# Kernel tuning notes

Measured on AMD Instinct MI355X. Metric: run time of the kernel, lower is better.

## Reference

```python
import jax, jax.numpy as jnp
import numpy as np


def setup_inputs() -> dict:
    key = jax.random.key(0)
    ks = jax.random.split(key, 5)
    B, T, S, D = 4, 32, 320, 768
    return {
        "x": jax.random.normal(ks[0], (B, T, S, D), dtype=jnp.float32),
        "qkv_w": jax.random.normal(ks[1], (D, 3 * D), dtype=jnp.float32) * 0.02,
        "qkv_b": jax.random.normal(ks[2], (3 * D,), dtype=jnp.float32) * 0.02,
        "out_w": jax.random.normal(ks[3], (D, D), dtype=jnp.float32) * 0.02,
        "out_b": jax.random.normal(ks[4], (D,), dtype=jnp.float32) * 0.02,
        "n_latents": 64,
        "n_heads": 12,
    }


def reference(x, qkv_w, qkv_b, out_w, out_b, n_latents, n_heads):
    B, T, S, D = x.shape
    H = n_heads
    hd = D // H
    scale = 1.0 / jnp.sqrt(jnp.asarray(hd, dtype=x.dtype))

    # qkv projection: [B,T,S,3D]
    qkv = jnp.einsum('btsd,de->btse', x, qkv_w) + qkv_b
    q, k, v = jnp.split(qkv, 3, axis=-1)
    # [B,T,S,H,hd]
    q = q.reshape(B, T, S, H, hd)
    k = k.reshape(B, T, S, H, hd)
    v = v.reshape(B, T, S, H, hd)

    # block-sparse mask: latent queries (rows < n_latents) cannot attend to
    # patch keys (cols >= n_latents); everything else allowed
    rows = jnp.arange(S) < n_latents          # latent query rows
    cols = jnp.arange(S) >= n_latents         # patch key cols
    allow = ~(rows[:, None] & cols[None, :])  # [S,S] bool

    # attention scores [B,T,H,Sq,Sk]
    scores = jnp.einsum('btqhd,btkhd->bthqk', q, k) * scale
    scores = jnp.where(allow, scores, -jnp.inf)
    attn = jax.nn.softmax(scores, axis=-1)

    y = jnp.einsum('bthqk,btkhd->btqhd', attn, v).reshape(B, T, S, D)
    return jnp.einsum('btsd,de->btse', y, out_w) + out_b
```

## Files before the change

kernel.cpp:

```cpp
#include <hip/hip_runtime.h>

typedef __attribute__((ext_vector_type(8))) short bf16x8;
typedef __attribute__((ext_vector_type(4))) float f32x4;
typedef __attribute__((ext_vector_type(16))) float f32x16;
typedef __attribute__((address_space(1))) void gvoid_t;
typedef __attribute__((address_space(3))) void lvoid_t;

#define DEVI __device__ __forceinline__
#define SB __builtin_amdgcn_sched_barrier(0)

DEVI unsigned short f2bf(float f) {
    unsigned int u = __builtin_bit_cast(unsigned int, f);
    u += 0x7fffu + ((u >> 16) & 1u);
    return (unsigned short)(u >> 16);
}

DEVI unsigned cvt_pk_bf16(float a, float b) {
    unsigned r;
    asm("v_cvt_pk_bf16_f32 %0, %1, %2" : "=v"(r) : "v"(a), "v"(b));
    return r;
}

DEVI f32x4 mfma16(bf16x8 a, bf16x8 b, f32x4 c) {
    return __builtin_amdgcn_mfma_f32_16x16x32_bf16(a, b, c, 0, 0, 0);
}

__global__ void k_convert(const float* __restrict__ in, unsigned short* __restrict__ out, int n8) {
    int i = blockIdx.x * 256 + threadIdx.x;
    if (i >= n8) return;
    const float4* p = (const float4*)in + (size_t)i * 2;
    float4 a = p[0], b = p[1];
    uint4 o;
    o.x = f2bf(a.x) | ((unsigned)f2bf(a.y) << 16);
    o.y = f2bf(a.z) | ((unsigned)f2bf(a.w) << 16);
    o.z = f2bf(b.x) | ((unsigned)f2bf(b.y) << 16);
    o.w = f2bf(b.z) | ((unsigned)f2bf(b.w) << 16);
    *((uint4*)out + i) = o;
}

__global__ void k_transpose(const float* __restrict__ w, unsigned short* __restrict__ wt, int K, int N) {
    __shared__ float tile[32][33];
    int n0 = blockIdx.x * 32, k0 = blockIdx.y * 32;
    int tx = threadIdx.x, ty = threadIdx.y;
#pragma unroll
    for (int r = 0; r < 32; r += 8)
        tile[ty + r][tx] = w[(size_t)(k0 + ty + r) * N + n0 + tx];
    __syncthreads();
#pragma unroll
    for (int r = 0; r < 32; r += 8)
        wt[(size_t)(n0 + ty + r) * K + k0 + tx] = f2bf(tile[tx][ty + r]);
}

__global__ __launch_bounds__(256) void k_kpack(const unsigned short* __restrict__ qkv,
                                               unsigned short* __restrict__ kp) {
    int bht = blockIdx.x;
    int t = bht % 10, bh = bht / 10;
    int h = bh % 12, bt = bh / 12;
    int c = threadIdx.x >> 6, l = threadIdx.x & 63;
    const unsigned short* src = qkv + (size_t)(bt * 320 + t * 32 + (l & 31)) * 2304
                                + 768 + h * 64 + c * 16 + (l >> 5) * 8;
    uint4 v = *(const uint4*)src;
    *(uint4*)(kp + ((size_t)bht * 4 + c) * 512 + l * 8) = v;
}

template <bool OUT_BF16>
__global__ __launch_bounds__(512, 2) void k_gemm256(const unsigned short* __restrict__ A,
                                                    const unsigned short* __restrict__ Bt,
                                                    const float* __restrict__ bias,
                                                    void* __restrict__ out,
                                                    int M, int N, int K) {
    __shared__ unsigned short smem[65536];

    const int tid = threadIdx.x;
    const int nwg = gridDim.x, bid = blockIdx.x;
    const int q8 = nwg >> 3, r8 = nwg & 7;
    const int xcd = bid & 7, lid = bid >> 3;
    const int swz = ((xcd < r8) ? xcd * (q8 + 1) : r8 * (q8 + 1) + (xcd - r8) * q8) + lid;
    const int ntn = N >> 8;
    const int bm = swz / ntn, bn = swz % ntn;

    const int lane = tid & 63, wid = tid >> 6;
    const int wr = wid >> 2, wc = wid & 3;
    const int lr = lane & 15, lg = lane >> 4;
    const int cswz = (lr & 7) << 3;
    const int col0 = (lg * 8) ^ cswz;

    const int NT = K >> 6;

    const int srowl = tid >> 3;
    const int scole = ((tid & 7) ^ (srowl & 7)) << 3;
    const unsigned short* aSrc = A  + (size_t)(bm * 256 + srowl) * K + scole;
    const unsigned short* bSrc = Bt + (size_t)(bn * 256 + srowl) * K + scole;

#define STG(matOff, srcBase, qq, koff, bufw)                                              \
    __builtin_amdgcn_global_load_lds((gvoid_t*)((srcBase) + (size_t)(qq) * 64 * K + (koff)), \
        (lvoid_t*)(smem + (matOff) + (bufw) * 16384 + (qq) * 4096 + tid * 8), 16, 0, 0)
#define LDA(mf, base, rowoff, kk) \
    *(const bf16x8*)((base) + ((rowoff) + (mf) * 16 + lr) * 64 + (col0 ^ ((kk) * 32)))

    f32x4 acc[8][4];
#pragma unroll
    for (int i = 0; i < 8; ++i)
#pragma unroll
        for (int j = 0; j < 4; ++j) acc[i][j] = (f32x4){0.f, 0.f, 0.f, 0.f};

    {
        const int k1 = (NT > 1) ? 64 : 0;
        STG(0, aSrc, 0, 0, 0); STG(0, aSrc, 1, 0, 0); STG(0, aSrc, 2, 0, 0); STG(0, aSrc, 3, 0, 0);
        STG(32768, bSrc, 0, 0, 0); STG(32768, bSrc, 1, 0, 0); STG(32768, bSrc, 2, 0, 0); STG(32768, bSrc, 3, 0, 0);
        STG(0, aSrc, 0, k1, 1); STG(0, aSrc, 2, k1, 1);
        asm volatile("s_waitcnt vmcnt(2)" ::: "memory");
        __builtin_amdgcn_s_barrier();
    }

#pragma unroll 1
    for (int t = 0; t < NT; ++t) {
        const int bufR = t & 1, bufW = bufR ^ 1;
        const int ko1 = (t + 1 < NT) ? (t + 1) * 64 : 0;
        const int ko2 = (t + 2 < NT) ? (t + 2) * 64 : 0;
        const unsigned short* abuf = smem + bufR * 16384;
        const unsigned short* bbuf = smem + 32768 + bufR * 16384;
        bf16x8 afv[4][2], b01[2][2], b23[2][2];

#pragma unroll
        for (int j = 0; j < 2; ++j)
#pragma unroll
            for (int kk = 0; kk < 2; ++kk)
                b01[j][kk] = LDA(j, bbuf, wc * 64, kk);
#pragma unroll
        for (int mf = 0; mf < 2; ++mf)
#pragma unroll
            for (int kk = 0; kk < 2; ++kk)
                afv[mf][kk] = LDA(mf, abuf, wr * 128, kk);
        SB;
#pragma unroll
        for (int mf = 2; mf < 4; ++mf)
#pragma unroll
            for (int kk = 0; kk < 2; ++kk)
                afv[mf][kk] = LDA(mf, abuf, wr * 128, kk);
        SB;
        STG(32768, bSrc, 0, ko1, bufW); STG(32768, bSrc, 1, ko1, bufW);
        asm volatile("s_waitcnt lgkmcnt(4)" ::: "memory"); SB;
        __builtin_amdgcn_s_setprio(1);
#pragma unroll
        for (int mf = 0; mf < 2; ++mf)
#pragma unroll
            for (int j = 0; j < 2; ++j)
#pragma unroll
                for (int kk = 0; kk < 2; ++kk)
                    acc[mf][j] = mfma16(afv[mf][kk], b01[j][kk], acc[mf][j]);
        __builtin_amdgcn_s_setprio(0);
        asm volatile("s_waitcnt lgkmcnt(0)" ::: "memory"); SB;
        __builtin_amdgcn_s_setprio(1);
#pragma unroll
        for (int mf = 2; mf < 4; ++mf)
#pragma unroll
            for (int j = 0; j < 2; ++j)
#pragma unroll
                for (int kk = 0; kk < 2; ++kk)
                    acc[mf][j] = mfma16(afv[mf][kk], b01[j][kk], acc[mf][j]);
        __builtin_amdgcn_s_setprio(0);

#pragma unroll
        for (int kk = 0; kk < 2; ++kk)
            b23[0][kk] = LDA(2, bbuf, wc * 64, kk);
        SB;
#pragma unroll
        for (int kk = 0; kk < 2; ++kk)
            b23[1][kk] = LDA(3, bbuf, wc * 64, kk);
        SB;
        STG(32768, bSrc, 2, ko1, bufW); STG(32768, bSrc, 3, ko1, bufW);
        asm volatile("s_waitcnt lgkmcnt(2)" ::: "memory"); SB;
        __builtin_amdgcn_s_setprio(1);
#pragma unroll
        for (int mf = 0; mf < 4; ++mf)
#pragma unroll
            for (int kk = 0; kk < 2; ++kk)
                acc[mf][2] = mfma16(afv[mf][kk], b23[0][kk], acc[mf][2]);
        __builtin_amdgcn_s_setprio(0);
        asm volatile("s_waitcnt lgkmcnt(0)" ::: "memory"); SB;
        __builtin_amdgcn_s_setprio(1);
#pragma unroll
        for (int mf = 0; mf < 4; ++mf)
#pragma unroll
            for (int kk = 0; kk < 2; ++kk)
                acc[mf][3] = mfma16(afv[mf][kk], b23[1][kk], acc[mf][3]);
        __builtin_amdgcn_s_setprio(0);

#pragma unroll
        for (int mf = 0; mf < 2; ++mf)
#pragma unroll
            for (int kk = 0; kk < 2; ++kk)
                afv[mf][kk] = LDA(mf, abuf, wr * 128 + 64, kk);
        SB;
#pragma unroll
        for (int mf = 2; mf < 4; ++mf)
#pragma unroll
            for (int kk = 0; kk < 2; ++kk)
                afv[mf][kk] = LDA(mf, abuf, wr * 128 + 64, kk);
        SB;
        STG(0, aSrc, 1, ko1, bufW); STG(0, aSrc, 3, ko1, bufW);
        asm volatile("s_waitcnt lgkmcnt(4)" ::: "memory"); SB;
        __builtin_amdgcn_s_setprio(1);
#pragma unroll
        for (int mf = 0; mf < 2; ++mf)
#pragma unroll
            for (int j = 0; j < 2; ++j)
#pragma unroll
                for (int kk = 0; kk < 2; ++kk)
                    acc[4 + mf][2 + j] = mfma16(afv[mf][kk], b23[j][kk], acc[4 + mf][2 + j]);
        __builtin_amdgcn_s_setprio(0);
        asm volatile("s_waitcnt lgkmcnt(0)" ::: "memory"); SB;
        __builtin_amdgcn_s_setprio(1);
#pragma unroll
        for (int mf = 2; mf < 4; ++mf)
#pragma unroll
            for (int j = 0; j < 2; ++j)
#pragma unroll
                for (int kk = 0; kk < 2; ++kk)
                    acc[4 + mf][2 + j] = mfma16(afv[mf][kk], b23[j][kk], acc[4 + mf][2 + j]);
        __builtin_amdgcn_s_setprio(0);

        __builtin_amdgcn_s_setprio(1);
#pragma unroll
        for (int mf = 0; mf < 4; ++mf)
#pragma unroll
            for (int j = 0; j < 2; ++j)
#pragma unroll
                for (int kk = 0; kk < 2; ++kk)
                    acc[4 + mf][j] = mfma16(afv[mf][kk], b01[j][kk], acc[4 + mf][j]);
        __builtin_amdgcn_s_setprio(0);
        asm volatile("s_waitcnt vmcnt(0)" ::: "memory");
        __builtin_amdgcn_s_barrier();
        STG(0, aSrc, 0, ko2, bufR); STG(0, aSrc, 2, ko2, bufR);
    }
#undef STG
#undef LDA

    asm volatile("s_waitcnt vmcnt(0)" ::: "memory");
    __syncthreads();
    float bv[4];
#pragma unroll
    for (int nf = 0; nf < 4; ++nf)
        bv[nf] = bias[bn * 256 + wc * 64 + nf * 16 + lr];

    if (OUT_BF16) {
        unsigned short* ebuf = smem + wid * 8192;
#pragma unroll
        for (int h = 0; h < 2; ++h) {
#pragma unroll
            for (int mf4 = 0; mf4 < 4; ++mf4) {
                int mf = h * 4 + mf4;
#pragma unroll
                for (int nf = 0; nf < 4; ++nf)
#pragma unroll
                    for (int i = 0; i < 4; ++i)
                        ebuf[(mf4 * 16 + lg * 4 + i) * 72 + nf * 16 + lr] = f2bf(acc[mf][nf][i] + bv[nf]);
            }
            asm volatile("s_waitcnt lgkmcnt(0)" ::: "memory"); SB;
#pragma unroll
            for (int ps = 0; ps < 8; ++ps) {
                int rl = ps * 8 + (lane >> 3), ck = lane & 7;
                uint4 vv = *(const uint4*)&ebuf[rl * 72 + ck * 8];
                int grow = bm * 256 + wr * 128 + h * 64 + rl;
                int gcol = bn * 256 + wc * 64 + ck * 8;
                *(uint4*)&((unsigned short*)out)[(size_t)grow * N + gcol] = vv;
            }
            asm volatile("s_waitcnt lgkmcnt(0)" ::: "memory"); SB;
        }
    } else {
        float* ebuf = (float*)smem + wid * 4096;
#pragma unroll
        for (int qq = 0; qq < 4; ++qq) {
#pragma unroll
            for (int m2 = 0; m2 < 2; ++m2) {
                int mf = qq * 2 + m2;
#pragma unroll
                for (int nf = 0; nf < 4; ++nf)
#pragma unroll
                    for (int i = 0; i < 4; ++i)
                        ebuf[(m2 * 16 + lg * 4 + i) * 68 + nf * 16 + lr] = acc[mf][nf][i] + bv[nf];
            }
            asm volatile("s_waitcnt lgkmcnt(0)" ::: "memory"); SB;
#pragma unroll
            for (int ps = 0; ps < 8; ++ps) {
                int rl = ps * 4 + (lane >> 4), ck = lane & 15;
                uint4 vv = *(const uint4*)&ebuf[rl * 68 + ck * 4];
                int grow = bm * 256 + wr * 128 + qq * 32 + rl;
                int gcol = bn * 256 + wc * 64 + ck * 4;
                *(uint4*)&((float*)out)[(size_t)grow * N + gcol] = vv;
            }
            asm volatile("s_waitcnt lgkmcnt(0)" ::: "memory"); SB;
        }
    }
}

__global__ __launch_bounds__(640) void k_attn5(const unsigned short* __restrict__ qkv,
                                               const unsigned short* __restrict__ kp,
                                               unsigned short* __restrict__ y) {
    int bt = blockIdx.x / 12, h = blockIdx.x % 12;
    const unsigned short* Qg = qkv + (size_t)bt * 320 * 2304 + h * 64;
    const unsigned short* Vg = Qg + 1536;
    const unsigned short* Kpb = kp + (size_t)blockIdx.x * 20480;

    __shared__ unsigned short Vt[10 * 64 * 40];

    int tid = threadIdx.x, w = tid >> 6, l = tid & 63;
    int q = l & 31, hh = l >> 5;
    int q0 = w * 32;
    int ntile = (w < 2) ? 2 : 10;

    {
        int k = tid >> 1;
        int tt = k >> 5, sk = k & 31;
        int d0 = (tid & 1) * 32;
        const unsigned short* src = Vg + (size_t)k * 2304 + d0;
#pragma unroll
        for (int c = 0; c < 4; ++c) {
            union { uint4 u; unsigned short s[8]; } vv;
            vv.u = *(const uint4*)(src + c * 8);
#pragma unroll
            for (int j = 0; j < 8; ++j) {
                int d = d0 + c * 8 + j;
                Vt[(tt * 64 + d) * 40 + (sk ^ (((d >> 3) & 3) << 3))] = vv.s[j];
            }
        }
    }

    bf16x8 qf[4];
#pragma unroll
    for (int c = 0; c < 4; ++c)
        qf[c] = *(const bf16x8*)(Qg + (size_t)(q0 + q) * 2304 + c * 16 + hh * 8);

    f32x16 o0 = (f32x16)0.f, o1 = (f32x16)0.f;
    float m = -3e38f, lsum = 0.f;
    const float SC = 0.125f * 1.44269504089f;

    bf16x8 kfA[4], kfB[4];
    auto loadK = [&](bf16x8 (&kf)[4], int tt) {
#pragma unroll
        for (int c = 0; c < 4; ++c)
            kf[c] = *(const bf16x8*)(Kpb + tt * 2048 + c * 512 + l * 8);
    };
    loadK(kfA, 0);

    __syncthreads();

    auto process = [&](int t, bf16x8 (&kf)[4]) {
        f32x16 sacc = (f32x16)0.f;
#pragma unroll
        for (int c = 0; c < 4; ++c)
            sacc = __builtin_amdgcn_mfma_f32_32x32x16_bf16(kf[c], qf[c], sacc, 0, 0, 0);

        float p[16];
#pragma unroll
        for (int r = 0; r < 16; ++r) p[r] = sacc[r] * SC;
        float tm = fmaxf(
            fmaxf(fmaxf(fmaxf(p[0], p[1]), fmaxf(p[2], p[3])),
                  fmaxf(fmaxf(p[4], p[5]), fmaxf(p[6], p[7]))),
            fmaxf(fmaxf(fmaxf(p[8], p[9]), fmaxf(p[10], p[11])),
                  fmaxf(fmaxf(p[12], p[13]), fmaxf(p[14], p[15]))));
        tm = fmaxf(tm, __shfl_xor(tm, 32));
        if (!__all(tm <= m + 8.f)) {
            float mn = fmaxf(m, tm);
            float al = __builtin_amdgcn_exp2f(m - mn);
            lsum *= al;
#pragma unroll
            for (int r = 0; r < 16; ++r) { o0[r] *= al; o1[r] *= al; }
            m = mn;
        }
#pragma unroll
        for (int r = 0; r < 16; ++r) p[r] = __builtin_amdgcn_exp2f(p[r] - m);
        float rs =
            ((p[0] + p[1]) + (p[2] + p[3])) + ((p[4] + p[5]) + (p[6] + p[7])) +
            (((p[8] + p[9]) + (p[10] + p[11])) + ((p[12] + p[13]) + (p[14] + p[15])));
        lsum += rs;

        unsigned a0 = cvt_pk_bf16(p[0], p[1]);
        unsigned a1 = cvt_pk_bf16(p[2], p[3]);
        unsigned b0 = cvt_pk_bf16(p[4], p[5]);
        unsigned b1 = cvt_pk_bf16(p[6], p[7]);
        asm("v_permlane32_swap_b32 %0, %1" : "+v"(a0), "+v"(b0));
        asm("v_permlane32_swap_b32 %0, %1" : "+v"(a1), "+v"(b1));
        unsigned c0 = cvt_pk_bf16(p[8], p[9]);
        unsigned c1 = cvt_pk_bf16(p[10], p[11]);
        unsigned d0 = cvt_pk_bf16(p[12], p[13]);
        unsigned d1 = cvt_pk_bf16(p[14], p[15]);
        asm("v_permlane32_swap_b32 %0, %1" : "+v"(c0), "+v"(d0));
        asm("v_permlane32_swap_b32 %0, %1" : "+v"(c1), "+v"(d1));
        union { unsigned u[4]; bf16x8 v; } pf0, pf1;
        pf0.u[0] = a0; pf0.u[1] = a1; pf0.u[2] = b0; pf0.u[3] = b1;
        pf1.u[0] = c0; pf1.u[1] = c1; pf1.u[2] = d0; pf1.u[3] = d1;

        const unsigned short* vt = Vt + t * 2560;
        {
            int d = q;
            int sw = (d >> 3) & 3;
            bf16x8 va0 = *(const bf16x8*)&vt[d * 40 + ((0 + hh) ^ sw) * 8];
            bf16x8 va1 = *(const bf16x8*)&vt[d * 40 + ((2 + hh) ^ sw) * 8];
            o0 = __builtin_amdgcn_mfma_f32_32x32x16_bf16(va0, pf0.v, o0, 0, 0, 0);
            o0 = __builtin_amdgcn_mfma_f32_32x32x16_bf16(va1, pf1.v, o0, 0, 0, 0);
        }
        {
            int d = 32 + q;
            int sw = (d >> 3) & 3;
            bf16x8 va0 = *(const bf16x8*)&vt[d * 40 + ((0 + hh) ^ sw) * 8];
            bf16x8 va1 = *(const bf16x8*)&vt[d * 40 + ((2 + hh) ^ sw) * 8];
            o1 = __builtin_amdgcn_mfma_f32_32x32x16_bf16(va0, pf0.v, o1, 0, 0, 0);
            o1 = __builtin_amdgcn_mfma_f32_32x32x16_bf16(va1, pf1.v, o1, 0, 0, 0);
        }
    };

    for (int t = 0; t < ntile; t += 2) {
        loadK(kfB, t + 1);
        process(t, kfA);
        loadK(kfA, (t + 2 < 10) ? (t + 2) : 8);
        process(t + 1, kfB);
    }

    lsum += __shfl_xor(lsum, 32);
    float inv = 1.f / lsum;
    unsigned short* yp = y + (size_t)(bt * 320 + q0 + q) * 768 + h * 64;
#pragma unroll
    for (int r = 0; r < 16; r += 2) {
        int dr = (r & 3) + 8 * (r >> 2) + 4 * hh;
        *(unsigned*)(yp + dr) =
            (unsigned)f2bf(o0[r] * inv) | ((unsigned)f2bf(o0[r + 1] * inv) << 16);
        *(unsigned*)(yp + 32 + dr) =
            (unsigned)f2bf(o1[r] * inv) | ((unsigned)f2bf(o1[r + 1] * inv) << 16);
    }
}

extern "C" void kernel_launch(void* const* d_in, const int* in_sizes, int n_in,
                              void* d_out, int out_size, void* d_ws, size_t ws_size,
                              hipStream_t stream) {
    const float* x     = (const float*)d_in[0];
    const float* qkv_w = (const float*)d_in[1];
    const float* qkv_b = (const float*)d_in[2];
    const float* out_w = (const float*)d_in[3];
    const float* out_b = (const float*)d_in[4];

    const int M = 40960;
    unsigned short* xb  = (unsigned short*)d_ws;
    unsigned short* w1t = xb + (size_t)M * 768;
    unsigned short* w2t = w1t + (size_t)2304 * 768;
    unsigned short* qkv = w2t + (size_t)768 * 768;
    unsigned short* yb  = qkv + (size_t)M * 2304;
    unsigned short* kp  = xb;

    k_convert<<<(M * 768 / 8 + 255) / 256, 256, 0, stream>>>(x, xb, M * 768 / 8);
    k_transpose<<<dim3(2304 / 32, 768 / 32), dim3(32, 8), 0, stream>>>(qkv_w, w1t, 768, 2304);
    k_transpose<<<dim3(768 / 32, 768 / 32), dim3(32, 8), 0, stream>>>(out_w, w2t, 768, 768);

    k_gemm256<true><<<(M / 256) * (2304 / 256), 512, 0, stream>>>(xb, w1t, qkv_b, (void*)qkv, M, 2304, 768);
    k_kpack<<<1536 * 10, 256, 0, stream>>>(qkv, kp);
    k_attn5<<<128 * 12, 640, 0, stream>>>(qkv, kp, yb);
    k_gemm256<false><<<(M / 256) * (768 / 256), 512, 0, stream>>>(yb, w2t, out_b, d_out, M, 768, 768);
}
```

Before: 378.3 us.

## Fuse fp32-to-bf16 conversion of x into the QKV GEMM A-tile loads

Removes the standalone conversion kernel. The QKV GEMM now reads fp32 activations straight from global memory into registers, converts them with packed bf16 conversion, and writes them into LDS, pipelined across the K loop. This avoids writing and re-reading a bf16 copy of x, but the A path loses the async global-to-LDS loads and adds VGPR pressure plus conversion ALU work inside the MFMA loop. The output GEMM also issues all of its B and A stage loads earlier in the iteration.

```diff
diff --git a/kernel.cpp b/kernel.cpp
--- a/kernel.cpp
+++ b/kernel.cpp
@@ -23,19 +23,6 @@
 
 DEVI f32x4 mfma16(bf16x8 a, bf16x8 b, f32x4 c) {
     return __builtin_amdgcn_mfma_f32_16x16x32_bf16(a, b, c, 0, 0, 0);
-}
-
-__global__ void k_convert(const float* __restrict__ in, unsigned short* __restrict__ out, int n8) {
-    int i = blockIdx.x * 256 + threadIdx.x;
-    if (i >= n8) return;
-    const float4* p = (const float4*)in + (size_t)i * 2;
-    float4 a = p[0], b = p[1];
-    uint4 o;
-    o.x = f2bf(a.x) | ((unsigned)f2bf(a.y) << 16);
-    o.y = f2bf(a.z) | ((unsigned)f2bf(a.w) << 16);
-    o.z = f2bf(b.x) | ((unsigned)f2bf(b.y) << 16);
-    o.w = f2bf(b.z) | ((unsigned)f2bf(b.w) << 16);
-    *((uint4*)out + i) = o;
 }
 
 __global__ void k_transpose(const float* __restrict__ w, unsigned short* __restrict__ wt, int K, int N) {
@@ -63,12 +50,11 @@
     *(uint4*)(kp + ((size_t)bht * 4 + c) * 512 + l * 8) = v;
 }
 
-template <bool OUT_BF16>
-__global__ __launch_bounds__(512, 2) void k_gemm256(const unsigned short* __restrict__ A,
-                                                    const unsigned short* __restrict__ Bt,
-                                                    const float* __restrict__ bias,
-                                                    void* __restrict__ out,
-                                                    int M, int N, int K) {
+__global__ __launch_bounds__(512, 2) void k_gemmF(const float* __restrict__ Af,
+                                                  const unsigned short* __restrict__ Bt,
+                                                  const float* __restrict__ bias,
+                                                  unsigned short* __restrict__ out,
+                                                  int M, int N, int K) {
     __shared__ unsigned short smem[65536];
 
     const int tid = threadIdx.x;
@@ -89,7 +75,239 @@
 
     const int srowl = tid >> 3;
     const int scole = ((tid & 7) ^ (srowl & 7)) << 3;
-    const unsigned short* aSrc = A  + (size_t)(bm * 256 + srowl) * K + scole;
+    const float* aF = Af + (size_t)(bm * 256 + srowl) * K + scole;
+    const unsigned short* bSrc = Bt + (size_t)(bn * 256 + srowl) * K + scole;
+
+#define STGB(qq, koff, bufw)                                                              \
+    __builtin_amdgcn_global_load_lds((gvoid_t*)(bSrc + (size_t)(qq) * 64 * K + (koff)),   \
+        (lvoid_t*)(smem + 32768 + (bufw) * 16384 + (qq) * 4096 + tid * 8), 16, 0, 0)
+#define LDA(mf, base, rowoff, kk) \
+    *(const bf16x8*)((base) + ((rowoff) + (mf) * 16 + lr) * 64 + (col0 ^ ((kk) * 32)))
+
+    f32x4 acc[8][4];
+#pragma unroll
+    for (int i = 0; i < 8; ++i)
+#pragma unroll
+        for (int j = 0; j < 4; ++j) acc[i][j] = (f32x4){0.f, 0.f, 0.f, 0.f};
+
+    float4 s0f, s1f, s2f, s3f;
+    auto loadA = [&](int qq0, int koff) {
+        const float* p0 = aF + (size_t)qq0 * 64 * K + koff;
+        const float* p1 = aF + (size_t)(qq0 + 1) * 64 * K + koff;
+        s0f = *(const float4*)(p0);
+        s1f = *(const float4*)(p0 + 4);
+        s2f = *(const float4*)(p1);
+        s3f = *(const float4*)(p1 + 4);
+    };
+    auto cvtwr = [&](int qq0, int bufw) {
+        union { unsigned u[4]; bf16x8 v; } pk;
+        pk.u[0] = cvt_pk_bf16(s0f.x, s0f.y);
+        pk.u[1] = cvt_pk_bf16(s0f.z, s0f.w);
+        pk.u[2] = cvt_pk_bf16(s1f.x, s1f.y);
+        pk.u[3] = cvt_pk_bf16(s1f.z, s1f.w);
+        *(bf16x8*)(smem + bufw * 16384 + qq0 * 4096 + tid * 8) = pk.v;
+        pk.u[0] = cvt_pk_bf16(s2f.x, s2f.y);
+        pk.u[1] = cvt_pk_bf16(s2f.z, s2f.w);
+        pk.u[2] = cvt_pk_bf16(s3f.x, s3f.y);
+        pk.u[3] = cvt_pk_bf16(s3f.z, s3f.w);
+        *(bf16x8*)(smem + bufw * 16384 + (qq0 + 1) * 4096 + tid * 8) = pk.v;
+    };
+
+    {
+        loadA(0, 0);
+        STGB(0, 0, 0); STGB(1, 0, 0); STGB(2, 0, 0); STGB(3, 0, 0);
+        asm volatile("s_waitcnt vmcnt(4)" ::: "memory");
+        cvtwr(0, 0);
+        loadA(2, 0);
+        asm volatile("s_waitcnt vmcnt(0)" ::: "memory");
+        cvtwr(2, 0);
+        asm volatile("s_waitcnt lgkmcnt(0)" ::: "memory");
+        __builtin_amdgcn_s_barrier();
+    }
+
+#pragma unroll 1
+    for (int t = 0; t < NT; ++t) {
+        const int bufR = t & 1, bufW = bufR ^ 1;
+        const int ko1 = (t + 1 < NT) ? (t + 1) * 64 : 0;
+        const unsigned short* abuf = smem + bufR * 16384;
+        const unsigned short* bbuf = smem + 32768 + bufR * 16384;
+        bf16x8 afv[4][2], b01[2][2], b23[2][2];
+
+#pragma unroll
+        for (int j = 0; j < 2; ++j)
+#pragma unroll
+            for (int kk = 0; kk < 2; ++kk)
+                b01[j][kk] = LDA(j, bbuf, wc * 64, kk);
+#pragma unroll
+        for (int mf = 0; mf < 2; ++mf)
+#pragma unroll
+            for (int kk = 0; kk < 2; ++kk)
+                afv[mf][kk] = LDA(mf, abuf, wr * 128, kk);
+        SB;
+#pragma unroll
+        for (int mf = 2; mf < 4; ++mf)
+#pragma unroll
+            for (int kk = 0; kk < 2; ++kk)
+                afv[mf][kk] = LDA(mf, abuf, wr * 128, kk);
+        SB;
+        loadA(0, ko1);
+        STGB(0, ko1, bufW); STGB(1, ko1, bufW);
+        STGB(2, ko1, bufW); STGB(3, ko1, bufW);
+        asm volatile("s_waitcnt lgkmcnt(4)" ::: "memory"); SB;
+        __builtin_amdgcn_s_setprio(1);
+#pragma unroll
+        for (int mf = 0; mf < 2; ++mf)
+#pragma unroll
+            for (int j = 0; j < 2; ++j)
+#pragma unroll
+                for (int kk = 0; kk < 2; ++kk)
+                    acc[mf][j] = mfma16(afv[mf][kk], b01[j][kk], acc[mf][j]);
+        __builtin_amdgcn_s_setprio(0);
+        asm volatile("s_waitcnt lgkmcnt(0)" ::: "memory"); SB;
+        __builtin_amdgcn_s_setprio(1);
+#pragma unroll
+        for (int mf = 2; mf < 4; ++mf)
+#pragma unroll
+            for (int j = 0; j < 2; ++j)
+#pragma unroll
+                for (int kk = 0; kk < 2; ++kk)
+                    acc[mf][j] = mfma16(afv[mf][kk], b01[j][kk], acc[mf][j]);
+        __builtin_amdgcn_s_setprio(0);
+
+#pragma unroll
+        for (int kk = 0; kk < 2; ++kk)
+            b23[0][kk] = LDA(2, bbuf, wc * 64, kk);
+        SB;
+#pragma unroll
+        for (int kk = 0; kk < 2; ++kk)
+            b23[1][kk] = LDA(3, bbuf, wc * 64, kk);
+        SB;
+        asm volatile("s_waitcnt vmcnt(4)" ::: "memory"); SB;
+        asm volatile("s_waitcnt lgkmcnt(2)" ::: "memory"); SB;
+        __builtin_amdgcn_s_setprio(1);
+#pragma unroll
+        for (int mf = 0; mf < 4; ++mf)
+#pragma unroll
+            for (int kk = 0; kk < 2; ++kk)
+                acc[mf][2] = mfma16(afv[mf][kk], b23[0][kk], acc[mf][2]);
+        __builtin_amdgcn_s_setprio(0);
+        cvtwr(0, bufW);
+        loadA(2, ko1);
+        asm volatile("s_waitcnt lgkmcnt(0)" ::: "memory"); SB;
+        __builtin_amdgcn_s_setprio(1);
+#pragma unroll
+        for (int mf = 0; mf < 4; ++mf)
+#pragma unroll
+            for (int kk = 0; kk < 2; ++kk)
+                acc[mf][3] = mfma16(afv[mf][kk], b23[1][kk], acc[mf][3]);
+        __builtin_amdgcn_s_setprio(0);
+
+#pragma unroll
+        for (int mf = 0; mf < 2; ++mf)
+#pragma unroll
+            for (int kk = 0; kk < 2; ++kk)
+                afv[mf][kk] = LDA(mf, abuf, wr * 128 + 64, kk);
+        SB;
+#pragma unroll
+        for (int mf = 2; mf < 4; ++mf)
+#pragma unroll
+            for (int kk = 0; kk < 2; ++kk)
+                afv[mf][kk] = LDA(mf, abuf, wr * 128 + 64, kk);
+        SB;
+        asm volatile("s_waitcnt lgkmcnt(4)" ::: "memory"); SB;
+        __builtin_amdgcn_s_setprio(1);
+#pragma unroll
+        for (int mf = 0; mf < 2; ++mf)
+#pragma unroll
+            for (int j = 0; j < 2; ++j)
+#pragma unroll
+                for (int kk = 0; kk < 2; ++kk)
+                    acc[4 + mf][2 + j] = mfma16(afv[mf][kk], b23[j][kk], acc[4 + mf][2 + j]);
+        __builtin_amdgcn_s_setprio(0);
+        asm volatile("s_waitcnt lgkmcnt(0)" ::: "memory"); SB;
+        __builtin_amdgcn_s_setprio(1);
+#pragma unroll
+        for (int mf = 2; mf < 4; ++mf)
+#pragma unroll
+            for (int j = 0; j < 2; ++j)
+#pragma unroll
+                for (int kk = 0; kk < 2; ++kk)
+                    acc[4 + mf][2 + j] = mfma16(afv[mf][kk], b23[j][kk], acc[4 + mf][2 + j]);
+        __builtin_amdgcn_s_setprio(0);
+
+        __builtin_amdgcn_s_setprio(1);
+#pragma unroll
+        for (int mf = 0; mf < 4; ++mf)
+#pragma unroll
+            for (int j = 0; j < 2; ++j)
+#pragma unroll
+                for (int kk = 0; kk < 2; ++kk)
+                    acc[4 + mf][j] = mfma16(afv[mf][kk], b01[j][kk], acc[4 + mf][j]);
+        __builtin_amdgcn_s_setprio(0);
+        asm volatile("s_waitcnt vmcnt(0)" ::: "memory");
+        cvtwr(2, bufW);
+        asm volatile("s_waitcnt lgkmcnt(0)" ::: "memory");
+        __builtin_amdgcn_s_barrier();
+    }
+#undef STGB
+#undef LDA
+
+    __syncthreads();
+    float bv[4];
+#pragma unroll
+    for (int nf = 0; nf < 4; ++nf)
+        bv[nf] = bias[bn * 256 + wc * 64 + nf * 16 + lr];
+    unsigned short* ebuf = smem + wid * 8192;
+#pragma unroll
+    for (int h = 0; h < 2; ++h) {
+#pragma unroll
+        for (int mf4 = 0; mf4 < 4; ++mf4) {
+            int mf = h * 4 + mf4;
+#pragma unroll
+            for (int nf = 0; nf < 4; ++nf)
+#pragma unroll
+                for (int i = 0; i < 4; ++i)
+                    ebuf[(mf4 * 16 + lg * 4 + i) * 72 + nf * 16 + lr] = f2bf(acc[mf][nf][i] + bv[nf]);
+        }
+        asm volatile("s_waitcnt lgkmcnt(0)" ::: "memory"); SB;
+#pragma unroll
+        for (int ps = 0; ps < 8; ++ps) {
+            int rl = ps * 8 + (lane >> 3), ck = lane & 7;
+            uint4 vv = *(const uint4*)&ebuf[rl * 72 + ck * 8];
+            int grow = bm * 256 + wr * 128 + h * 64 + rl;
+            int gcol = bn * 256 + wc * 64 + ck * 8;
+            *(uint4*)&out[(size_t)grow * N + gcol] = vv;
+        }
+        asm volatile("s_waitcnt lgkmcnt(0)" ::: "memory"); SB;
+    }
+}
+
+__global__ __launch_bounds__(512, 2) void k_gemm2(const unsigned short* __restrict__ A,
+                                                  const unsigned short* __restrict__ Bt,
+                                                  const float* __restrict__ bias,
+                                                  float* __restrict__ out,
+                                                  int M, int N, int K) {
+    __shared__ unsigned short smem[65536];
+
+    const int tid = threadIdx.x;
+    const int nwg = gridDim.x, bid = blockIdx.x;
+    const int q8 = nwg >> 3, r8 = nwg & 7;
+    const int xcd = bid & 7, lid = bid >> 3;
+    const int swz = ((xcd < r8) ? xcd * (q8 + 1) : r8 * (q8 + 1) + (xcd - r8) * q8) + lid;
+    const int ntn = N >> 8;
+    const int bm = swz / ntn, bn = swz % ntn;
+
+    const int lane = tid & 63, wid = tid >> 6;
+    const int wr = wid >> 2, wc = wid & 3;
+    const int lr = lane & 15, lg = lane >> 4;
+    const int cswz = (lr & 7) << 3;
+    const int col0 = (lg * 8) ^ cswz;
+
+    const int NT = K >> 6;
+
+    const int srowl = tid >> 3;
+    const int scole = ((tid & 7) ^ (srowl & 7)) << 3;
+    const unsigned short* aSrc = A + (size_t)(bm * 256 + srowl) * K + scole;
     const unsigned short* bSrc = Bt + (size_t)(bn * 256 + srowl) * K + scole;
 
 #define STG(matOff, srcBase, qq, koff, bufw)                                              \
@@ -140,6 +358,8 @@
                 afv[mf][kk] = LDA(mf, abuf, wr * 128, kk);
         SB;
         STG(32768, bSrc, 0, ko1, bufW); STG(32768, bSrc, 1, ko1, bufW);
+        STG(32768, bSrc, 2, ko1, bufW); STG(32768, bSrc, 3, ko1, bufW);
+        STG(0, aSrc, 1, ko1, bufW); STG(0, aSrc, 3, ko1, bufW);
         asm volatile("s_waitcnt lgkmcnt(4)" ::: "memory"); SB;
         __builtin_amdgcn_s_setprio(1);
 #pragma unroll
@@ -169,7 +389,6 @@
         for (int kk = 0; kk < 2; ++kk)
             b23[1][kk] = LDA(3, bbuf, wc * 64, kk);
         SB;
-        STG(32768, bSrc, 2, ko1, bufW); STG(32768, bSrc, 3, ko1, bufW);
         asm volatile("s_waitcnt lgkmcnt(2)" ::: "memory"); SB;
         __builtin_amdgcn_s_setprio(1);
 #pragma unroll
@@ -199,7 +418,6 @@
             for (int kk = 0; kk < 2; ++kk)
                 afv[mf][kk] = LDA(mf, abuf, wr * 128 + 64, kk);
         SB;
-        STG(0, aSrc, 1, ko1, bufW); STG(0, aSrc, 3, ko1, bufW);
         asm volatile("s_waitcnt lgkmcnt(4)" ::: "memory"); SB;
         __builtin_amdgcn_s_setprio(1);
 #pragma unroll
@@ -243,55 +461,28 @@
 #pragma unroll
     for (int nf = 0; nf < 4; ++nf)
         bv[nf] = bias[bn * 256 + wc * 64 + nf * 16 + lr];
-
-    if (OUT_BF16) {
-        unsigned short* ebuf = smem + wid * 8192;
-#pragma unroll
-        for (int h = 0; h < 2; ++h) {
-#pragma unroll
-            for (int mf4 = 0; mf4 < 4; ++mf4) {
-                int mf = h * 4 + mf4;
-#pragma unroll
-                for (int nf = 0; nf < 4; ++nf)
-#pragma unroll
-                    for (int i = 0; i < 4; ++i)
-                        ebuf[(mf4 * 16 + lg * 4 + i) * 72 + nf * 16 + lr] = f2bf(acc[mf][nf][i] + bv[nf]);
-            }
-            asm volatile("s_waitcnt lgkmcnt(0)" ::: "memory"); SB;
-#pragma unroll
-            for (int ps = 0; ps < 8; ++ps) {
-                int rl = ps * 8 + (lane >> 3), ck = lane & 7;
-                uint4 vv = *(const uint4*)&ebuf[rl * 72 + ck * 8];
-                int grow = bm * 256 + wr * 128 + h * 64 + rl;
-                int gcol = bn * 256 + wc * 64 + ck * 8;
-                *(uint4*)&((unsigned short*)out)[(size_t)grow * N + gcol] = vv;
-            }
-            asm volatile("s_waitcnt lgkmcnt(0)" ::: "memory"); SB;
-        }
-    } else {
-        float* ebuf = (float*)smem + wid * 4096;
-#pragma unroll
-        for (int qq = 0; qq < 4; ++qq) {
-#pragma unroll
-            for (int m2 = 0; m2 < 2; ++m2) {
-                int mf = qq * 2 + m2;
-#pragma unroll
-                for (int nf = 0; nf < 4; ++nf)
-#pragma unroll
-                    for (int i = 0; i < 4; ++i)
-                        ebuf[(m2 * 16 + lg * 4 + i) * 68 + nf * 16 + lr] = acc[mf][nf][i] + bv[nf];
-            }
-            asm volatile("s_waitcnt lgkmcnt(0)" ::: "memory"); SB;
-#pragma unroll
-            for (int ps = 0; ps < 8; ++ps) {
-                int rl = ps * 4 + (lane >> 4), ck = lane & 15;
-                uint4 vv = *(const uint4*)&ebuf[rl * 68 + ck * 4];
-                int grow = bm * 256 + wr * 128 + qq * 32 + rl;
-                int gcol = bn * 256 + wc * 64 + ck * 4;
-                *(uint4*)&((float*)out)[(size_t)grow * N + gcol] = vv;
-            }
-            asm volatile("s_waitcnt lgkmcnt(0)" ::: "memory"); SB;
-        }
+    float* ebuf = (float*)smem + wid * 4096;
+#pragma unroll
+    for (int qq = 0; qq < 4; ++qq) {
+#pragma unroll
+        for (int m2 = 0; m2 < 2; ++m2) {
+            int mf = qq * 2 + m2;
+#pragma unroll
+            for (int nf = 0; nf < 4; ++nf)
+#pragma unroll
+                for (int i = 0; i < 4; ++i)
+                    ebuf[(m2 * 16 + lg * 4 + i) * 68 + nf * 16 + lr] = acc[mf][nf][i] + bv[nf];
+        }
+        asm volatile("s_waitcnt lgkmcnt(0)" ::: "memory"); SB;
+#pragma unroll
+        for (int ps = 0; ps < 8; ++ps) {
+            int rl = ps * 4 + (lane >> 4), ck = lane & 15;
+            uint4 vv = *(const uint4*)&ebuf[rl * 68 + ck * 4];
+            int grow = bm * 256 + wr * 128 + qq * 32 + rl;
+            int gcol = bn * 256 + wc * 64 + ck * 4;
+            *(uint4*)&out[(size_t)grow * N + gcol] = vv;
+        }
+        asm volatile("s_waitcnt lgkmcnt(0)" ::: "memory"); SB;
     }
 }
 
@@ -441,19 +632,17 @@
     const float* out_b = (const float*)d_in[4];
 
     const int M = 40960;
-    unsigned short* xb  = (unsigned short*)d_ws;
-    unsigned short* w1t = xb + (size_t)M * 768;
+    unsigned short* w1t = (unsigned short*)d_ws;
     unsigned short* w2t = w1t + (size_t)2304 * 768;
     unsigned short* qkv = w2t + (size_t)768 * 768;
     unsigned short* yb  = qkv + (size_t)M * 2304;
-    unsigned short* kp  = xb;
-
-    k_convert<<<(M * 768 / 8 + 255) / 256, 256, 0, stream>>>(x, xb, M * 768 / 8);
+    unsigned short* kp  = yb + (size_t)M * 768;
+
     k_transpose<<<dim3(2304 / 32, 768 / 32), dim3(32, 8), 0, stream>>>(qkv_w, w1t, 768, 2304);
     k_transpose<<<dim3(768 / 32, 768 / 32), dim3(32, 8), 0, stream>>>(out_w, w2t, 768, 768);
 
-    k_gemm256<true><<<(M / 256) * (2304 / 256), 512, 0, stream>>>(xb, w1t, qkv_b, (void*)qkv, M, 2304, 768);
+    k_gemmF<<<(M / 256) * (2304 / 256), 512, 0, stream>>>(x, w1t, qkv_b, qkv, M, 2304, 768);
     k_kpack<<<1536 * 10, 256, 0, stream>>>(qkv, kp);
     k_attn5<<<128 * 12, 640, 0, stream>>>(qkv, kp, yb);
-    k_gemm256<false><<<(M / 256) * (768 / 256), 512, 0, stream>>>(yb, w2t, out_b, d_out, M, 768, 768);
-}
+    k_gemm2<<<(M / 256) * (768 / 256), 512, 0, stream>>>(yb, w2t, out_b, (float*)d_out, M, 768, 768);
+}
```

After: 429.9 us. 13.6% more time.
